# Kernel tuning notes

Measured on AMD Instinct MI355X. Metric: run time of the kernel, lower is better.

## Reference

```python
import jax, jax.numpy as jnp
import numpy as np
from jax import lax

B_, L_ = 2, 512
D_MODEL, EXPAND, HEAD_DIM, NGROUPS, D_STATE, D_CONV = 512, 2, 64, 1, 64, 3
D_INNER = EXPAND * D_MODEL            # 1024
NHEADS = D_INNER // HEAD_DIM          # 16
CONV_DIM = D_INNER + 2 * NGROUPS * D_STATE   # 1152
D_IN_PROJ = 2 * D_INNER + 2 * NGROUPS * D_STATE + NHEADS  # 2192
RMS_EPS = 1e-5


def silu(x):
    return x * jax.nn.sigmoid(x)


def segsum(x):
    # x: (..., T) -> (..., T, T); out[..., i, j] = sum_{j<k<=i} x[..., k], -inf above diag
    T = x.shape[-1]
    xr = jnp.broadcast_to(x[..., None], x.shape + (T,))
    keep = jnp.tril(jnp.ones((T, T), dtype=bool), -1)
    xr = jnp.where(keep, xr, 0.0)
    s = jnp.cumsum(xr, axis=-2)
    diag = jnp.tril(jnp.ones((T, T), dtype=bool), 0)
    return jnp.where(diag, s, -jnp.inf)


def ssd(x, A, Bm, Cm, chunk):
    # x: (b,l,h,p), A: (b,l,h), Bm/Cm: (b,l,g,n); chunk==1 as in the source forward
    b, l, h, p = x.shape
    c = l // chunk
    n = Bm.shape[-1]
    x = x.reshape(b, c, chunk, h, p)
    Bm = Bm.reshape(b, c, chunk, Bm.shape[2], n)
    Cm = Cm.reshape(b, c, chunk, Cm.shape[2], n)
    A = A.reshape(b, c, chunk, h).transpose(0, 3, 1, 2)        # (b,h,c,l)
    A_cumsum = jnp.cumsum(A, axis=-1)
    Lmat = jnp.exp(segsum(A))                                   # (b,h,c,l,l)
    # broadcast group dim (g==1) to heads, matching torch.einsum broadcasting
    Bb = jnp.broadcast_to(Bm, (b, c, chunk, h, n))
    Cb = jnp.broadcast_to(Cm, (b, c, chunk, h, n))
    Y_diag = jnp.einsum('bclhn,bcshn,bhcls,bcshp->bclhp', Cb, Bb, Lmat, x)
    decay_states = jnp.exp(A_cumsum[:, :, :, -1:] - A_cumsum)   # (b,h,c,l)
    states = jnp.einsum('bclhn,bhcl,bclhp->bchpn', Bb, decay_states, x)
    states = jnp.concatenate([jnp.zeros_like(states[:, :1]), states], axis=1)  # (b,c+1,h,p,n)
    A_last = jnp.pad(A_cumsum[:, :, :, -1], ((0, 0), (0, 0), (1, 0)))          # (b,h,c+1)
    decay_chunk = jnp.exp(segsum(A_last))                       # (b,h,c+1,c+1)
    new_states = jnp.einsum('bhzc,bchpn->bzhpn', decay_chunk, states)
    states = new_states[:, :-1]                                 # (b,c,h,p,n)
    state_decay_out = jnp.exp(A_cumsum)
    Y_off = jnp.einsum('bclhn,bchpn,bhcl->bclhp', Cb, states, state_decay_out)
    return (Y_diag + Y_off).reshape(b, l, h, p)


def causal_dwconv(x, w, bias):
    # x: (B,L,C); w: (C,K) depthwise; torch pads (K-1) both sides then slices [:L] == left-pad only
    xt = x.transpose(0, 2, 1)
    y = lax.conv_general_dilated(xt, w[:, None, :], (1,), [(D_CONV - 1, 0)],
                                 feature_group_count=CONV_DIM,
                                 dimension_numbers=('NCH', 'OIH', 'NCH'))
    return y.transpose(0, 2, 1) + bias


def setup_inputs() -> dict:
    key = jax.random.key(0)
    ks = jax.random.split(key, 8)
    u = jax.random.normal(ks[0], (B_, L_, D_MODEL), dtype=jnp.float32)
    W_in = jax.random.normal(ks[1], (D_MODEL, D_IN_PROJ), dtype=jnp.float32) / np.sqrt(D_MODEL).astype(np.float32)
    conv_w = jax.random.normal(ks[2], (CONV_DIM, D_CONV), dtype=jnp.float32) * 0.3
    conv_b = jnp.zeros((CONV_DIM,), dtype=jnp.float32)
    dt = jnp.exp(jax.random.uniform(ks[3], (NHEADS,), dtype=jnp.float32)
                 * (np.float32(np.log(0.1)) - np.float32(np.log(0.001))) + np.float32(np.log(0.001)))
    dt = jnp.clip(dt, 1e-4, None)
    dt_bias = dt + jnp.log(-jnp.expm1(-dt))
    A_log = jnp.log(jax.random.uniform(ks[4], (NHEADS,), dtype=jnp.float32, minval=1.0, maxval=16.0))
    D_param = jnp.ones((NHEADS,), dtype=jnp.float32)
    rms_w = jnp.ones((D_INNER,), dtype=jnp.float32)
    W_out = jax.random.normal(ks[5], (D_INNER, D_MODEL), dtype=jnp.float32) / np.sqrt(D_INNER).astype(np.float32)
    return {"u": u, "W_in": W_in, "conv_w": conv_w, "conv_b": conv_b, "dt_bias": dt_bias,
            "A_log": A_log, "D_param": D_param, "rms_w": rms_w, "W_out": W_out}


def reference(u, W_in, conv_w, conv_b, dt_bias, A_log, D_param, rms_w, W_out):
    b, l, _ = u.shape
    zxbcdt = u @ W_in                                   # (b,l,D_IN_PROJ)
    z = zxbcdt[..., :D_INNER]
    xBC = zxbcdt[..., D_INNER:D_INNER + CONV_DIM]
    dt = zxbcdt[..., D_INNER + CONV_DIM:]
    dt = jax.nn.softplus(dt + dt_bias)                  # (b,l,h)
    A = -jnp.exp(A_log)                                 # (h,)
    xBC = silu(causal_dwconv(xBC, conv_w, conv_b))      # (b,l,CONV_DIM)
    x = xBC[..., :D_INNER].reshape(b, l, NHEADS, HEAD_DIM)
    Bm = xBC[..., D_INNER:D_INNER + D_STATE][:, :, None, :]     # (b,l,1,n)
    Cm = xBC[..., D_INNER + D_STATE:][:, :, None, :]            # (b,l,1,n)
    y = ssd(x * dt[..., None], A * dt, Bm, Cm, 1)       # (b,l,h,p)
    y = y + x * D_param[:, None]
    y = y.reshape(b, l, D_INNER)
    # gated RMSNorm
    yz = y * silu(z)
    y = yz * lax.rsqrt(jnp.mean(yz * yz, axis=-1, keepdims=True) + RMS_EPS) * rms_w
    return y @ W_out
```

## Files before the change

### kernel.cpp

```cpp
#include <hip/hip_runtime.h>
#include <hip/hip_bf16.h>

#define B_SZ 2
#define L_SZ 512
#define D_MODEL 512
#define D_INNER 1024
#define HEAD_DIM 64
#define NHEADS 16
#define D_STATE 64
#define D_CONV 3
#define CONV_DIM 1152
#define D_IN_PROJ 2192
#define BL (B_SZ * L_SZ)
#define RMS_EPS 1e-5f
#define QC 64
#define NCH 8
#define NPAD1 2304
#define PB 72

typedef __attribute__((ext_vector_type(8))) short short8t;
typedef __attribute__((ext_vector_type(8))) unsigned short ushort8t;
typedef __attribute__((ext_vector_type(4))) unsigned short ushort4t;
typedef __attribute__((ext_vector_type(4))) float f32x4;

__device__ __forceinline__ unsigned short f2bf(float f) {
    unsigned u = __float_as_uint(f);
    u += 0x7fff + ((u >> 16) & 1);
    return (unsigned short)(u >> 16);
}
__device__ __forceinline__ float bf2f(unsigned short u) {
    return __uint_as_float(((unsigned)u) << 16);
}

__device__ __forceinline__ void gload_lds16(const void* g, void* lds) {
    __builtin_amdgcn_global_load_lds(
        (const __attribute__((address_space(1))) unsigned int*)g,
        (__attribute__((address_space(3))) unsigned int*)lds, 16, 0, 0);
}

__device__ __forceinline__ void transpose_tile_bf16(const float* __restrict__ src,
                                                    unsigned short* __restrict__ dst,
                                                    int K, int Nin, int tile, int ntn) {
    __shared__ float T[64][65];
    int tid = threadIdx.x;
    int nt = tile % ntn, kt = tile / ntn;
    int n0 = nt * 64, k0 = kt * 64;
#pragma unroll
    for (int rr = 0; rr < 4; ++rr) {
        int k = k0 + (tid >> 4) + rr * 16;
        int nn = (tid & 15) * 4;
#pragma unroll
        for (int q = 0; q < 4; ++q) {
            int n = n0 + nn + q;
            T[(tid >> 4) + rr * 16][nn + q] = (n < Nin) ? src[(size_t)k * Nin + n] : 0.f;
        }
    }
    __syncthreads();
    int nn2 = tid >> 2, kc = tid & 3;
    unsigned short ov[16];
#pragma unroll
    for (int j = 0; j < 16; ++j) ov[j] = f2bf(T[kc * 16 + j][nn2]);
    unsigned short* p = dst + (size_t)(n0 + nn2) * K + k0 + kc * 16;
    *(ushort8t*)p = *(ushort8t*)&ov[0];
    *(ushort8t*)(p + 8) = *(ushort8t*)&ov[8];
}

__global__ __launch_bounds__(256) void prep_kernel(const float* __restrict__ W_in,
                                                   const float* __restrict__ W_out,
                                                   const float* __restrict__ u,
                                                   unsigned short* __restrict__ Wt1,
                                                   unsigned short* __restrict__ Wt2,
                                                   unsigned short* __restrict__ u_bf) {
    int bid = blockIdx.x;
    if (bid < 288) {
        transpose_tile_bf16(W_in, Wt1, D_MODEL, D_IN_PROJ, bid, 36);
    } else if (bid < 416) {
        transpose_tile_bf16(W_out, Wt2, D_INNER, D_MODEL, bid - 288, 8);
    } else {
        int i = ((bid - 416) * 256 + threadIdx.x) * 8;
        float4 v0 = *(const float4*)(u + i);
        float4 v1 = *(const float4*)(u + i + 4);
        unsigned short ov[8] = {f2bf(v0.x), f2bf(v0.y), f2bf(v0.z), f2bf(v0.w),
                                f2bf(v1.x), f2bf(v1.y), f2bf(v1.z), f2bf(v1.w)};
        *(ushort8t*)(u_bf + i) = *(ushort8t*)&ov[0];
    }
}

__global__ __launch_bounds__(256) void gemm_in(const unsigned short* __restrict__ A,
                                               const unsigned short* __restrict__ Bt,
                                               float* __restrict__ C,
                                               unsigned short* __restrict__ xbc,
                                               float* __restrict__ dtb) {
    const int K = D_MODEL;
    __shared__ char sm[49152];
    int tid = threadIdx.x;
    int w = tid >> 6, l = tid & 63;
    int m0 = blockIdx.y * 64, n0 = blockIdx.x * 64;
    int wm = w >> 1, wn = w & 1;

    f32x4 acc[2][2];
#pragma unroll
    for (int i = 0; i < 2; ++i)
#pragma unroll
        for (int j = 0; j < 2; ++j) acc[i][j] = (f32x4){0.f, 0.f, 0.f, 0.f};

    auto stage = [&](const unsigned short* src, int row0, int k0, char* dst) {
#pragma unroll
        for (int p = 0; p < 2; ++p) {
            int c = w * 2 + p;
            int row = c * 8 + (l >> 3);
            int scb = ((l & 7) << 4) ^ ((row & 7) << 4);
            gload_lds16(src + (size_t)(row0 + row) * K + k0 + (scb >> 1), dst + c * 1024);
        }
    };

    const int nkt = K / 64;
    stage(A, m0, 0, sm);
    stage(Bt, n0, 0, sm + 8192);
    stage(A, m0, 64, sm + 16384);
    stage(Bt, n0, 64, sm + 16384 + 8192);

    for (int kt = 0; kt < nkt; ++kt) {
        if (kt + 2 < nkt) {
            char* d = sm + ((kt + 2) % 3) * 16384;
            stage(A, m0, (kt + 2) * 64, d);
            stage(Bt, n0, (kt + 2) * 64, d + 8192);
        }
        int inflight = nkt - 1 - kt;
        if (inflight >= 2)      asm volatile("s_waitcnt vmcnt(8)" ::: "memory");
        else if (inflight == 1) asm volatile("s_waitcnt vmcnt(4)" ::: "memory");
        else                    asm volatile("s_waitcnt vmcnt(0)" ::: "memory");
        __builtin_amdgcn_s_barrier();

        const char* Ab = sm + (kt % 3) * 16384;
        const char* Bb = Ab + 8192;
#pragma unroll
        for (int kk = 0; kk < 2; ++kk) {
            short8t af[2], bf[2];
#pragma unroll
            for (int i = 0; i < 2; ++i) {
                int r = wm * 32 + i * 16 + (l & 15);
                int cb = (kk * 64 + (l >> 4) * 16) ^ ((r & 7) << 4);
                af[i] = *(const short8t*)(Ab + r * 128 + cb);
            }
#pragma unroll
            for (int j = 0; j < 2; ++j) {
                int r = wn * 32 + j * 16 + (l & 15);
                int cb = (kk * 64 + (l >> 4) * 16) ^ ((r & 7) << 4);
                bf[j] = *(const short8t*)(Bb + r * 128 + cb);
            }
#pragma unroll
            for (int i = 0; i < 2; ++i)
#pragma unroll
                for (int j = 0; j < 2; ++j)
                    acc[i][j] = __builtin_amdgcn_mfma_f32_16x16x32_bf16(af[i], bf[j], acc[i][j], 0, 0, 0);
        }
        __builtin_amdgcn_s_barrier();
    }

#pragma unroll
    for (int i = 0; i < 2; ++i)
#pragma unroll
        for (int j = 0; j < 2; ++j) {
            int row = m0 + wm * 32 + i * 16 + (l >> 4) * 4;
            int col = n0 + wn * 32 + j * 16 + (l & 15);
#pragma unroll
            for (int r = 0; r < 4; ++r) {
                float v = acc[i][j][r];
                int rr = row + r;
                if (col < D_INNER) {
                    C[(size_t)rr * D_IN_PROJ + col] = v;
                } else if (col < D_INNER + CONV_DIM) {
                    xbc[(size_t)rr * CONV_DIM + (col - D_INNER)] = f2bf(v);
                } else if (col < D_IN_PROJ) {
                    dtb[(size_t)rr * 16 + (col - D_INNER - CONV_DIM)] = v;
                }
            }
        }
}

__device__ __forceinline__ float4 conv4b(const unsigned short* __restrict__ xrow,
                                         int gl, int ch,
                                         const float* __restrict__ conv_w,
                                         const float* __restrict__ conv_b) {
    ushort4t u2 = *(const ushort4t*)(xrow + ch);
    ushort4t u1 = {0, 0, 0, 0}, u0 = {0, 0, 0, 0};
    if (gl >= 1) u1 = *(const ushort4t*)(xrow + ch - CONV_DIM);
    if (gl >= 2) u0 = *(const ushort4t*)(xrow + ch - 2 * CONV_DIM);
    float4 o;
    float a;
    a = conv_b[ch+0] + conv_w[(ch+0)*3]*bf2f(u0[0]) + conv_w[(ch+0)*3+1]*bf2f(u1[0]) + conv_w[(ch+0)*3+2]*bf2f(u2[0]);
    o.x = a / (1.f + __expf(-a));
    a = conv_b[ch+1] + conv_w[(ch+1)*3]*bf2f(u0[1]) + conv_w[(ch+1)*3+1]*bf2f(u1[1]) + conv_w[(ch+1)*3+2]*bf2f(u2[1]);
    o.y = a / (1.f + __expf(-a));
    a = conv_b[ch+2] + conv_w[(ch+2)*3]*bf2f(u0[2]) + conv_w[(ch+2)*3+1]*bf2f(u1[2]) + conv_w[(ch+2)*3+2]*bf2f(u2[2]);
    o.z = a / (1.f + __expf(-a));
    a = conv_b[ch+3] + conv_w[(ch+3)*3]*bf2f(u0[3]) + conv_w[(ch+3)*3+1]*bf2f(u1[3]) + conv_w[(ch+3)*3+2]*bf2f(u2[3]);
    o.w = a / (1.f + __expf(-a));
    return o;
}

__global__ __launch_bounds__(256) void ssd_passA(const unsigned short* __restrict__ xbc,
                                                 const float* __restrict__ dtb,
                                                 const float* __restrict__ conv_w,
                                                 const float* __restrict__ conv_b,
                                                 const float* __restrict__ dt_bias,
                                                 const float* __restrict__ A_log,
                                                 const float* __restrict__ D_param,
                                                 float* __restrict__ y,
                                                 float* __restrict__ Zbuf,
                                                 float* __restrict__ Ebuf) {
    int blk = blockIdx.x;
    int h = blk & 15;
    int c = (blk >> 4) & 7;
    int b = blk >> 7;
    int tid = threadIdx.x;

    __shared__ __align__(16) unsigned short Cs_bf[QC][PB];
    __shared__ __align__(16) unsigned short Bs_bf[QC][PB];
    __shared__ __align__(16) unsigned short XDT_bf[QC][PB];
    __shared__ __align__(16) unsigned short BTw_bf[QC][PB];
    __shared__ float csh[QC], dts[QC], wh[QC];
#define PS_bf Cs_bf

    int bl0 = b * L_SZ + c * QC;

    if (tid < 64) {
        int t = tid;
        float draw = dtb[(size_t)(bl0 + t) * 16 + h];
        float dtv = draw + dt_bias[h];
        dtv = (dtv > 20.f) ? dtv : log1pf(expf(dtv));
        float A = -expf(A_log[h]);
        float cs = A * dtv;
#pragma unroll
        for (int off = 1; off < 64; off <<= 1) {
            float tmp = __shfl_up(cs, off);
            if (t >= off) cs += tmp;
        }
        float cs63 = __shfl(cs, 63);
        dts[t] = dtv;
        csh[t] = cs;
        wh[t] = __expf(cs63 - cs);
        Ebuf[(((size_t)(b * NHEADS + h) * NCH) + c) * QC + t] = __expf(cs);
    }

    int row16 = tid >> 4;
    int col4 = (tid & 15) * 4;
#pragma unroll
    for (int r = 0; r < 4; ++r) {
        int t = r * 16 + row16;
        int gl = c * QC + t;
        const unsigned short* xrow = xbc + (size_t)(bl0 + t) * CONV_DIM;
        float4 Bv = conv4b(xrow, gl, D_INNER + col4, conv_w, conv_b);
        float4 Cv = conv4b(xrow, gl, D_INNER + D_STATE + col4, conv_w, conv_b);
        ushort4t bq = {f2bf(Bv.x), f2bf(Bv.y), f2bf(Bv.z), f2bf(Bv.w)};
        ushort4t cq = {f2bf(Cv.x), f2bf(Cv.y), f2bf(Cv.z), f2bf(Cv.w)};
        *(ushort4t*)&Bs_bf[t][col4] = bq;
        *(ushort4t*)&Cs_bf[t][col4] = cq;
    }
    __syncthreads();

#pragma unroll
    for (int r = 0; r < 4; ++r) {
        int t = r * 16 + row16;
        int gl = c * QC + t;
        const unsigned short* xrow = xbc + (size_t)(bl0 + t) * CONV_DIM;
        float4 xv = conv4b(xrow, gl, h * HEAD_DIM + col4, conv_w, conv_b);
        float d = dts[t], wt = wh[t];
        xv.x *= d; xv.y *= d; xv.z *= d; xv.w *= d;
        ushort4t xq = {f2bf(xv.x), f2bf(xv.y), f2bf(xv.z), f2bf(xv.w)};
        ushort4t bq = *(ushort4t*)&Bs_bf[t][col4];
#pragma unroll
        for (int q = 0; q < 4; ++q) {
            int ch = col4 + q;
            int f8 = ((ch >> 2) & 7) << 3;
            XDT_bf[ch][t ^ f8] = xq[q];
            BTw_bf[ch][t ^ f8] = f2bf(bf2f(bq[q]) * wt);
        }
    }
    __syncthreads();

    int l = tid & 63, wv = tid >> 6;
    int wm = wv >> 1, wn = wv & 1;
    int fr = l & 15, fq = l >> 4;

    f32x4 g[2][2];
    {
#pragma unroll
        for (int i = 0; i < 2; ++i)
#pragma unroll
            for (int j = 0; j < 2; ++j) g[i][j] = (f32x4){0.f, 0.f, 0.f, 0.f};
#pragma unroll
        for (int kk = 0; kk < 2; ++kk) {
            short8t af[2], bb[2];
#pragma unroll
            for (int i = 0; i < 2; ++i)
                af[i] = *(const short8t*)&Cs_bf[wm * 32 + i * 16 + fr][kk * 32 + fq * 8];
#pragma unroll
            for (int j = 0; j < 2; ++j)
                bb[j] = *(const short8t*)&Bs_bf[wn * 32 + j * 16 + fr][kk * 32 + fq * 8];
#pragma unroll
            for (int i = 0; i < 2; ++i)
#pragma unroll
                for (int j = 0; j < 2; ++j)
                    g[i][j] = __builtin_amdgcn_mfma_f32_16x16x32_bf16(af[i], bb[j], g[i][j], 0, 0, 0);
        }
    }
    __syncthreads();

    {
#pragma unroll
        for (int i = 0; i < 2; ++i)
#pragma unroll
            for (int j = 0; j < 2; ++j) {
                int s = wn * 32 + j * 16 + fr;
                float css = csh[s];
#pragma unroll
                for (int r = 0; r < 4; ++r) {
                    int t = wm * 32 + i * 16 + fq * 4 + r;
                    float v = (s <= t) ? g[i][j][r] * __expf(csh[t] - css) : 0.f;
                    PS_bf[t][s] = f2bf(v);
                }
            }
    }
    __syncthreads();

    {
        f32x4 yv[2][2];
#pragma unroll
        for (int i = 0; i < 2; ++i)
#pragma unroll
            for (int j = 0; j < 2; ++j) yv[i][j] = (f32x4){0.f, 0.f, 0.f, 0.f};
#pragma unroll
        for (int kk = 0; kk < 2; ++kk) {
            short8t af[2], bb[2];
            int K0 = kk * 32 + fq * 8;
#pragma unroll
            for (int i = 0; i < 2; ++i)
                af[i] = *(const short8t*)&PS_bf[wm * 32 + i * 16 + fr][K0];
#pragma unroll
            for (int j = 0; j < 2; ++j) {
                int r = wn * 32 + j * 16 + fr;
                bb[j] = *(const short8t*)&XDT_bf[r][K0 ^ (((r >> 2) & 7) << 3)];
            }
#pragma unroll
            for (int i = 0; i < 2; ++i)
#pragma unroll
                for (int j = 0; j < 2; ++j)
                    yv[i][j] = __builtin_amdgcn_mfma_f32_16x16x32_bf16(af[i], bb[j], yv[i][j], 0, 0, 0);
        }
        float Dp = D_param[h];
#pragma unroll
        for (int i = 0; i < 2; ++i)
#pragma unroll
            for (int j = 0; j < 2; ++j) {
                int p = wn * 32 + j * 16 + fr;
                int f8 = ((p >> 2) & 7) << 3;
#pragma unroll
                for (int r = 0; r < 4; ++r) {
                    int t = wm * 32 + i * 16 + fq * 4 + r;
                    float xval = bf2f(XDT_bf[p][t ^ f8]);
                    float fct = Dp / dts[t];
                    y[(size_t)(bl0 + t) * D_INNER + h * HEAD_DIM + p] =
                        yv[i][j][r] + fct * xval;
                }
            }
    }

    {
        f32x4 zv[2][2];
#pragma unroll
        for (int i = 0; i < 2; ++i)
#pragma unroll
            for (int j = 0; j < 2; ++j) zv[i][j] = (f32x4){0.f, 0.f, 0.f, 0.f};
#pragma unroll
        for (int kk = 0; kk < 2; ++kk) {
            short8t af[2], bb[2];
            int K0 = kk * 32 + fq * 8;
#pragma unroll
            for (int i = 0; i < 2; ++i) {
                int r = wm * 32 + i * 16 + fr;
                af[i] = *(const short8t*)&XDT_bf[r][K0 ^ (((r >> 2) & 7) << 3)];
            }
#pragma unroll
            for (int j = 0; j < 2; ++j) {
                int r = wn * 32 + j * 16 + fr;
                bb[j] = *(const short8t*)&BTw_bf[r][K0 ^ (((r >> 2) & 7) << 3)];
            }
#pragma unroll
            for (int i = 0; i < 2; ++i)
#pragma unroll
                for (int j = 0; j < 2; ++j)
                    zv[i][j] = __builtin_amdgcn_mfma_f32_16x16x32_bf16(af[i], bb[j], zv[i][j], 0, 0, 0);
        }
        float* Zr = Zbuf + (((size_t)(b * NHEADS + h) * NCH) + c) * (HEAD_DIM * D_STATE);
#pragma unroll
        for (int i = 0; i < 2; ++i)
#pragma unroll
            for (int j = 0; j < 2; ++j) {
                int n = wn * 32 + j * 16 + fr;
#pragma unroll
                for (int r = 0; r < 4; ++r) {
                    int p = wm * 32 + i * 16 + fq * 4 + r;
                    Zr[p * D_STATE + n] = zv[i][j][r];
                }
            }
    }
#undef PS_bf
}

__global__ __launch_bounds__(256) void ssd_passC(const unsigned short* __restrict__ xbc,
                                                 const float* __restrict__ conv_w,
                                                 const float* __restrict__ conv_b,
                                                 const float* __restrict__ Zbuf,
                                                 const float* __restrict__ Ebuf,
                                                 float* __restrict__ y) {
    int blk = blockIdx.x;
    int h = blk & 15;
    int q = blk >> 4;
    int c = 1 + (q % 7);
    int b = q / 7;
    int tid = threadIdx.x;

    __shared__ __align__(16) unsigned short Cs_bf[QC][PB];
    __shared__ __align__(16) unsigned short S_bf[QC][PB];
    __shared__ float Eh[QC];

    int bl0 = b * L_SZ + c * QC;
    const float* Zb = Zbuf + ((size_t)(b * NHEADS + h) * NCH) * (HEAD_DIM * D_STATE);
    const float* Eb = Ebuf + ((size_t)(b * NHEADS + h) * NCH) * QC;

    {
        int p = tid >> 2, nq = (tid & 3) * 16;
        float S16[16];
#pragma unroll
        for (int qq = 0; qq < 16; ++qq) S16[qq] = 0.f;
        float wgt = 1.f;
        for (int j = c - 1; j >= 0; --j) {
            const float* Zj = Zb + (size_t)j * (HEAD_DIM * D_STATE) + p * D_STATE + nq;
#pragma unroll
            for (int q4 = 0; q4 < 4; ++q4) {
                float4 z = *(const float4*)(Zj + q4 * 4);
                S16[q4 * 4 + 0] += wgt * z.x;
                S16[q4 * 4 + 1] += wgt * z.y;
                S16[q4 * 4 + 2] += wgt * z.z;
                S16[q4 * 4 + 3] += wgt * z.w;
            }
            wgt *= Eb[(size_t)j * QC + 63];
        }
#pragma unroll
        for (int q4 = 0; q4 < 4; ++q4) {
            ushort4t s4 = {f2bf(S16[q4 * 4 + 0]), f2bf(S16[q4 * 4 + 1]),
                           f2bf(S16[q4 * 4 + 2]), f2bf(S16[q4 * 4 + 3])};
            *(ushort4t*)&S_bf[p][nq + q4 * 4] = s4;
        }
    }

    int row16 = tid >> 4, col4 = (tid & 15) * 4;
#pragma unroll
    for (int r = 0; r < 4; ++r) {
        int t = r * 16 + row16;
        int gl = c * QC + t;
        const unsigned short* xrow = xbc + (size_t)(bl0 + t) * CONV_DIM;
        float4 Cv = conv4b(xrow, gl, D_INNER + D_STATE + col4, conv_w, conv_b);
        ushort4t cq = {f2bf(Cv.x), f2bf(Cv.y), f2bf(Cv.z), f2bf(Cv.w)};
        *(ushort4t*)&Cs_bf[t][col4] = cq;
    }
    if (tid < 64)
        Eh[tid] = Ebuf[(((size_t)(b * NHEADS + h) * NCH) + c) * QC + tid];
    __syncthreads();

    int l = tid & 63, wv = tid >> 6;
    int wm = wv >> 1, wn = wv & 1;
    int fr = l & 15, fq = l >> 4;
    f32x4 acc[2][2];
#pragma unroll
    for (int i = 0; i < 2; ++i)
#pragma unroll
        for (int j = 0; j < 2; ++j) acc[i][j] = (f32x4){0.f, 0.f, 0.f, 0.f};
#pragma unroll
    for (int kk = 0; kk < 2; ++kk) {
        short8t af[2], bb[2];
#pragma unroll
        for (int i = 0; i < 2; ++i)
            af[i] = *(const short8t*)&Cs_bf[wm * 32 + i * 16 + fr][kk * 32 + fq * 8];
#pragma unroll
        for (int j = 0; j < 2; ++j)
            bb[j] = *(const short8t*)&S_bf[wn * 32 + j * 16 + fr][kk * 32 + fq * 8];
#pragma unroll
        for (int i = 0; i < 2; ++i)
#pragma unroll
            for (int j = 0; j < 2; ++j)
                acc[i][j] = __builtin_amdgcn_mfma_f32_16x16x32_bf16(af[i], bb[j], acc[i][j], 0, 0, 0);
    }
#pragma unroll
    for (int i = 0; i < 2; ++i)
#pragma unroll
        for (int j = 0; j < 2; ++j) {
            int p = wn * 32 + j * 16 + fr;
#pragma unroll
            for (int r = 0; r < 4; ++r) {
                int t = wm * 32 + i * 16 + fq * 4 + r;
                float* yp = y + (size_t)(bl0 + t) * D_INNER + h * HEAD_DIM + p;
                *yp += Eh[t] * acc[i][j][r];
            }
        }
}

__global__ __launch_bounds__(256) void gated_rmsnorm_kernel(const float* __restrict__ zxbcdt,
                                                            const float* __restrict__ y,
                                                            const float* __restrict__ rms_w,
                                                            unsigned short* __restrict__ yn_bf) {
    int bl = blockIdx.x;
    int tid = threadIdx.x;
    __shared__ float red[4];
    __shared__ float sscale;
    float vals[4];
    float sumsq = 0.f;
#pragma unroll
    for (int i = 0; i < 4; ++i) {
        int col = tid + i * 256;
        float yv = y[(size_t)bl * D_INNER + col];
        float z = zxbcdt[(size_t)bl * D_IN_PROJ + col];
        float yz = yv * (z / (1.f + expf(-z)));
        vals[i] = yz;
        sumsq += yz * yz;
    }
#pragma unroll
    for (int off = 32; off; off >>= 1) sumsq += __shfl_xor(sumsq, off);
    int wave = tid >> 6, lane = tid & 63;
    if (lane == 0) red[wave] = sumsq;
    __syncthreads();
    if (tid == 0) {
        float t = red[0] + red[1] + red[2] + red[3];
        sscale = rsqrtf(t / (float)D_INNER + RMS_EPS);
    }
    __syncthreads();
    float sc = sscale;
#pragma unroll
    for (int i = 0; i < 4; ++i) {
        int col = tid + i * 256;
        yn_bf[(size_t)bl * D_INNER + col] = f2bf(vals[i] * sc * rms_w[col]);
    }
}

__global__ __launch_bounds__(256) void gemm_mfma32(const unsigned short* __restrict__ A,
                                                   const unsigned short* __restrict__ Bt,
                                                   float* __restrict__ C,
                                                   int N, int K) {
    __shared__ char sm[36864];
    int tid = threadIdx.x;
    int w = tid >> 6, l = tid & 63;
    int m0 = blockIdx.y * 32, n0 = blockIdx.x * 64;
    int wm = w >> 1, wn = w & 1;

    f32x4 acc[2];
    acc[0] = (f32x4){0.f, 0.f, 0.f, 0.f};
    acc[1] = (f32x4){0.f, 0.f, 0.f, 0.f};

    auto stageA = [&](int k0, char* dst) {
        int row = w * 8 + (l >> 3);
        int scb = ((l & 7) << 4) ^ ((row & 7) << 4);
        gload_lds16(A + (size_t)(m0 + row) * K + k0 + (scb >> 1), dst + w * 1024);
    };
    auto stageB = [&](int k0, char* dst) {
#pragma unroll
        for (int p = 0; p < 2; ++p) {
            int c = w * 2 + p;
            int row = c * 8 + (l >> 3);
            int scb = ((l & 7) << 4) ^ ((row & 7) << 4);
            gload_lds16(Bt + (size_t)(n0 + row) * K + k0 + (scb >> 1), dst + c * 1024);
        }
    };

    int nkt = K / 64;
    stageA(0, sm); stageB(0, sm + 4096);
    stageA(64, sm + 12288); stageB(64, sm + 12288 + 4096);

    for (int kt = 0; kt < nkt; ++kt) {
        if (kt + 2 < nkt) {
            char* d = sm + ((kt + 2) % 3) * 12288;
            stageA((kt + 2) * 64, d);
            stageB((kt + 2) * 64, d + 4096);
        }
        int inflight = nkt - 1 - kt;
        if (inflight >= 2)      asm volatile("s_waitcnt vmcnt(6)" ::: "memory");
        else if (inflight == 1) asm volatile("s_waitcnt vmcnt(3)" ::: "memory");
        else                    asm volatile("s_waitcnt vmcnt(0)" ::: "memory");
        __builtin_amdgcn_s_barrier();

        const char* Ab = sm + (kt % 3) * 12288;
        const char* Bb = Ab + 4096;
#pragma unroll
        for (int kk = 0; kk < 2; ++kk) {
            short8t af;
            {
                int r = wm * 16 + (l & 15);
                int cb = (kk * 64 + (l >> 4) * 16) ^ ((r & 7) << 4);
                af = *(const short8t*)(Ab + r * 128 + cb);
            }
#pragma unroll
            for (int j = 0; j < 2; ++j) {
                int r = wn * 32 + j * 16 + (l & 15);
                int cb = (kk * 64 + (l >> 4) * 16) ^ ((r & 7) << 4);
                short8t bfv = *(const short8t*)(Bb + r * 128 + cb);
                acc[j] = __builtin_amdgcn_mfma_f32_16x16x32_bf16(af, bfv, acc[j], 0, 0, 0);
            }
        }
        __builtin_amdgcn_s_barrier();
    }

#pragma unroll
    for (int j = 0; j < 2; ++j) {
        int col = n0 + wn * 32 + j * 16 + (l & 15);
        int rowb = m0 + wm * 16 + (l >> 4) * 4;
#pragma unroll
        for (int r = 0; r < 4; ++r)
            C[(size_t)(rowb + r) * N + col] = acc[j][r];
    }
}

extern "C" void kernel_launch(void* const* d_in, const int* in_sizes, int n_in,
                              void* d_out, int out_size, void* d_ws, size_t ws_size,
                              hipStream_t stream) {
    const float* u       = (const float*)d_in[0];
    const float* W_in    = (const float*)d_in[1];
    const float* conv_w  = (const float*)d_in[2];
    const float* conv_b  = (const float*)d_in[3];
    const float* dt_bias = (const float*)d_in[4];
    const float* A_log   = (const float*)d_in[5];
    const float* D_param = (const float*)d_in[6];
    const float* rms_w   = (const float*)d_in[7];
    const float* W_out   = (const float*)d_in[8];
    float* out = (float*)d_out;

    float* ws = (float*)d_ws;
    float* zxbcdt = ws;
    float* y      = zxbcdt + (size_t)BL * D_IN_PROJ;
    float* Zbuf   = y + (size_t)BL * D_INNER;
    float* Ebuf   = Zbuf + (size_t)32 * NCH * 4096;
    float* dtb    = Ebuf + (size_t)32 * NCH * QC;
    unsigned short* u_bf  = (unsigned short*)(dtb + (size_t)BL * 16);
    unsigned short* Wt1   = u_bf + (size_t)BL * D_MODEL;
    unsigned short* Wt2   = Wt1 + (size_t)NPAD1 * D_MODEL;
    unsigned short* yn_bf = Wt2 + (size_t)D_MODEL * D_INNER;
    unsigned short* xbc   = yn_bf + (size_t)BL * D_INNER;

    prep_kernel<<<672, 256, 0, stream>>>(W_in, W_out, u, Wt1, Wt2, u_bf);

    gemm_in<<<dim3(NPAD1 / 64, BL / 64), 256, 0, stream>>>(
        u_bf, Wt1, zxbcdt, xbc, dtb);

    ssd_passA<<<B_SZ * NCH * NHEADS, 256, 0, stream>>>(
        xbc, dtb, conv_w, conv_b, dt_bias, A_log, D_param, y, Zbuf, Ebuf);
    ssd_passC<<<224, 256, 0, stream>>>(xbc, conv_w, conv_b, Zbuf, Ebuf, y);

    gated_rmsnorm_kernel<<<BL, 256, 0, stream>>>(zxbcdt, y, rms_w, yn_bf);

    gemm_mfma32<<<dim3(D_MODEL / 64, BL / 32), 256, 0, stream>>>(
        yn_bf, Wt2, out, D_MODEL, D_INNER);
}
```

Measured before the change: 47.19 us.

## Fuse gated RMSNorm into SSD epilogues and output GEMM row scaling

Removes the standalone gated RMSNorm kernel. The SSD pass epilogues now compute y*silu(z), write it as bf16 and emit per-head partial sums of squares. The output GEMM reduces those partials into a per-row rsqrt scale, and rms_w is folded into the transposed W_out during prep. This drops one launch and one full read/write of y, at the cost of extra z loads and reductions inside the SSD kernels and a small reduction in the GEMM epilogue.

```diff
diff --git a/kernel.cpp b/kernel.cpp
--- a/kernel.cpp
+++ b/kernel.cpp
@@ -39,6 +39,7 @@
 }
 
 __device__ __forceinline__ void transpose_tile_bf16(const float* __restrict__ src,
+                                                    const float* __restrict__ scale,
                                                     unsigned short* __restrict__ dst,
                                                     int K, int Nin, int tile, int ntn) {
     __shared__ float T[64][65];
@@ -48,11 +49,12 @@
 #pragma unroll
     for (int rr = 0; rr < 4; ++rr) {
         int k = k0 + (tid >> 4) + rr * 16;
+        float sc = scale ? scale[k] : 1.f;
         int nn = (tid & 15) * 4;
 #pragma unroll
         for (int q = 0; q < 4; ++q) {
             int n = n0 + nn + q;
-            T[(tid >> 4) + rr * 16][nn + q] = (n < Nin) ? src[(size_t)k * Nin + n] : 0.f;
+            T[(tid >> 4) + rr * 16][nn + q] = (n < Nin) ? src[(size_t)k * Nin + n] * sc : 0.f;
         }
     }
     __syncthreads();
@@ -67,15 +69,16 @@
 
 __global__ __launch_bounds__(256) void prep_kernel(const float* __restrict__ W_in,
                                                    const float* __restrict__ W_out,
+                                                   const float* __restrict__ rms_w,
                                                    const float* __restrict__ u,
                                                    unsigned short* __restrict__ Wt1,
                                                    unsigned short* __restrict__ Wt2,
                                                    unsigned short* __restrict__ u_bf) {
     int bid = blockIdx.x;
     if (bid < 288) {
-        transpose_tile_bf16(W_in, Wt1, D_MODEL, D_IN_PROJ, bid, 36);
+        transpose_tile_bf16(W_in, nullptr, Wt1, D_MODEL, D_IN_PROJ, bid, 36);
     } else if (bid < 416) {
-        transpose_tile_bf16(W_out, Wt2, D_INNER, D_MODEL, bid - 288, 8);
+        transpose_tile_bf16(W_out, rms_w, Wt2, D_INNER, D_MODEL, bid - 288, 8);
     } else {
         int i = ((bid - 416) * 256 + threadIdx.x) * 8;
         float4 v0 = *(const float4*)(u + i);
@@ -200,14 +203,19 @@
     return o;
 }
 
+__device__ __forceinline__ float silu(float z) { return z / (1.f + __expf(-z)); }
+
 __global__ __launch_bounds__(256) void ssd_passA(const unsigned short* __restrict__ xbc,
                                                  const float* __restrict__ dtb,
+                                                 const float* __restrict__ zx,
                                                  const float* __restrict__ conv_w,
                                                  const float* __restrict__ conv_b,
                                                  const float* __restrict__ dt_bias,
                                                  const float* __restrict__ A_log,
                                                  const float* __restrict__ D_param,
                                                  float* __restrict__ y,
+                                                 unsigned short* __restrict__ yz_bf,
+                                                 float* __restrict__ psum,
                                                  float* __restrict__ Zbuf,
                                                  float* __restrict__ Ebuf) {
     int blk = blockIdx.x;
@@ -221,6 +229,7 @@
     __shared__ __align__(16) unsigned short XDT_bf[QC][PB];
     __shared__ __align__(16) unsigned short BTw_bf[QC][PB];
     __shared__ float csh[QC], dts[QC], wh[QC];
+    __shared__ float sq_lds[QC][2];
 #define PS_bf Cs_bf
 
     int bl0 = b * L_SZ + c * QC;
@@ -350,21 +359,57 @@
                     yv[i][j] = __builtin_amdgcn_mfma_f32_16x16x32_bf16(af[i], bb[j], yv[i][j], 0, 0, 0);
         }
         float Dp = D_param[h];
-#pragma unroll
-        for (int i = 0; i < 2; ++i)
-#pragma unroll
-            for (int j = 0; j < 2; ++j) {
-                int p = wn * 32 + j * 16 + fr;
-                int f8 = ((p >> 2) & 7) << 3;
+        if (c == 0) {
+            float sloc[2][4] = {{0.f, 0.f, 0.f, 0.f}, {0.f, 0.f, 0.f, 0.f}};
+#pragma unroll
+            for (int i = 0; i < 2; ++i)
+#pragma unroll
+                for (int j = 0; j < 2; ++j) {
+                    int p = wn * 32 + j * 16 + fr;
+                    int f8 = ((p >> 2) & 7) << 3;
+#pragma unroll
+                    for (int r = 0; r < 4; ++r) {
+                        int t = wm * 32 + i * 16 + fq * 4 + r;
+                        float xval = bf2f(XDT_bf[p][t ^ f8]);
+                        float yval = yv[i][j][r] + (Dp / dts[t]) * xval;
+                        float z = zx[(size_t)(bl0 + t) * D_IN_PROJ + h * HEAD_DIM + p];
+                        float yz = yval * silu(z);
+                        yz_bf[(size_t)(bl0 + t) * D_INNER + h * HEAD_DIM + p] = f2bf(yz);
+                        sloc[i][r] += yz * yz;
+                    }
+                }
+#pragma unroll
+            for (int i = 0; i < 2; ++i)
 #pragma unroll
                 for (int r = 0; r < 4; ++r) {
-                    int t = wm * 32 + i * 16 + fq * 4 + r;
-                    float xval = bf2f(XDT_bf[p][t ^ f8]);
-                    float fct = Dp / dts[t];
-                    y[(size_t)(bl0 + t) * D_INNER + h * HEAD_DIM + p] =
-                        yv[i][j][r] + fct * xval;
+                    float v = sloc[i][r];
+                    v += __shfl_xor(v, 1); v += __shfl_xor(v, 2);
+                    v += __shfl_xor(v, 4); v += __shfl_xor(v, 8);
+                    if (fr == 0) {
+                        int t = wm * 32 + i * 16 + fq * 4 + r;
+                        sq_lds[t][wn] = v;
+                    }
                 }
-            }
+            __syncthreads();
+            if (tid < 64)
+                psum[(size_t)(bl0 + tid) * 16 + h] = sq_lds[tid][0] + sq_lds[tid][1];
+        } else {
+#pragma unroll
+            for (int i = 0; i < 2; ++i)
+#pragma unroll
+                for (int j = 0; j < 2; ++j) {
+                    int p = wn * 32 + j * 16 + fr;
+                    int f8 = ((p >> 2) & 7) << 3;
+#pragma unroll
+                    for (int r = 0; r < 4; ++r) {
+                        int t = wm * 32 + i * 16 + fq * 4 + r;
+                        float xval = bf2f(XDT_bf[p][t ^ f8]);
+                        float fct = Dp / dts[t];
+                        y[(size_t)(bl0 + t) * D_INNER + h * HEAD_DIM + p] =
+                            yv[i][j][r] + fct * xval;
+                    }
+                }
+        }
     }
 
     {
@@ -410,11 +455,14 @@
 }
 
 __global__ __launch_bounds__(256) void ssd_passC(const unsigned short* __restrict__ xbc,
+                                                 const float* __restrict__ zx,
                                                  const float* __restrict__ conv_w,
                                                  const float* __restrict__ conv_b,
                                                  const float* __restrict__ Zbuf,
                                                  const float* __restrict__ Ebuf,
-                                                 float* __restrict__ y) {
+                                                 const float* __restrict__ y,
+                                                 unsigned short* __restrict__ yz_bf,
+                                                 float* __restrict__ psum) {
     int blk = blockIdx.x;
     int h = blk & 15;
     int q = blk >> 4;
@@ -425,6 +473,7 @@
     __shared__ __align__(16) unsigned short Cs_bf[QC][PB];
     __shared__ __align__(16) unsigned short S_bf[QC][PB];
     __shared__ float Eh[QC];
+    __shared__ float sq_lds[QC][2];
 
     int bl0 = b * L_SZ + c * QC;
     const float* Zb = Zbuf + ((size_t)(b * NHEADS + h) * NCH) * (HEAD_DIM * D_STATE);
@@ -493,6 +542,8 @@
             for (int j = 0; j < 2; ++j)
                 acc[i][j] = __builtin_amdgcn_mfma_f32_16x16x32_bf16(af[i], bb[j], acc[i][j], 0, 0, 0);
     }
+
+    float sloc[2][4] = {{0.f, 0.f, 0.f, 0.f}, {0.f, 0.f, 0.f, 0.f}};
 #pragma unroll
     for (int i = 0; i < 2; ++i)
 #pragma unroll
@@ -501,54 +552,38 @@
 #pragma unroll
             for (int r = 0; r < 4; ++r) {
                 int t = wm * 32 + i * 16 + fq * 4 + r;
-                float* yp = y + (size_t)(bl0 + t) * D_INNER + h * HEAD_DIM + p;
-                *yp += Eh[t] * acc[i][j][r];
-            }
-        }
-}
-
-__global__ __launch_bounds__(256) void gated_rmsnorm_kernel(const float* __restrict__ zxbcdt,
-                                                            const float* __restrict__ y,
-                                                            const float* __restrict__ rms_w,
-                                                            unsigned short* __restrict__ yn_bf) {
-    int bl = blockIdx.x;
-    int tid = threadIdx.x;
-    __shared__ float red[4];
-    __shared__ float sscale;
-    float vals[4];
-    float sumsq = 0.f;
-#pragma unroll
-    for (int i = 0; i < 4; ++i) {
-        int col = tid + i * 256;
-        float yv = y[(size_t)bl * D_INNER + col];
-        float z = zxbcdt[(size_t)bl * D_IN_PROJ + col];
-        float yz = yv * (z / (1.f + expf(-z)));
-        vals[i] = yz;
-        sumsq += yz * yz;
-    }
-#pragma unroll
-    for (int off = 32; off; off >>= 1) sumsq += __shfl_xor(sumsq, off);
-    int wave = tid >> 6, lane = tid & 63;
-    if (lane == 0) red[wave] = sumsq;
+                size_t idx = (size_t)(bl0 + t) * D_INNER + h * HEAD_DIM + p;
+                float yval = y[idx] + Eh[t] * acc[i][j][r];
+                float z = zx[(size_t)(bl0 + t) * D_IN_PROJ + h * HEAD_DIM + p];
+                float yz = yval * silu(z);
+                yz_bf[idx] = f2bf(yz);
+                sloc[i][r] += yz * yz;
+            }
+        }
+#pragma unroll
+    for (int i = 0; i < 2; ++i)
+#pragma unroll
+        for (int r = 0; r < 4; ++r) {
+            float v = sloc[i][r];
+            v += __shfl_xor(v, 1); v += __shfl_xor(v, 2);
+            v += __shfl_xor(v, 4); v += __shfl_xor(v, 8);
+            if (fr == 0) {
+                int t = wm * 32 + i * 16 + fq * 4 + r;
+                sq_lds[t][wn] = v;
+            }
+        }
     __syncthreads();
-    if (tid == 0) {
-        float t = red[0] + red[1] + red[2] + red[3];
-        sscale = rsqrtf(t / (float)D_INNER + RMS_EPS);
-    }
-    __syncthreads();
-    float sc = sscale;
-#pragma unroll
-    for (int i = 0; i < 4; ++i) {
-        int col = tid + i * 256;
-        yn_bf[(size_t)bl * D_INNER + col] = f2bf(vals[i] * sc * rms_w[col]);
-    }
-}
-
-__global__ __launch_bounds__(256) void gemm_mfma32(const unsigned short* __restrict__ A,
-                                                   const unsigned short* __restrict__ Bt,
-                                                   float* __restrict__ C,
-                                                   int N, int K) {
+    if (tid < 64)
+        psum[(size_t)(bl0 + tid) * 16 + h] = sq_lds[tid][0] + sq_lds[tid][1];
+}
+
+__global__ __launch_bounds__(256) void gemm_out(const unsigned short* __restrict__ A,
+                                                const unsigned short* __restrict__ Bt,
+                                                const float* __restrict__ psum,
+                                                float* __restrict__ C) {
+    const int N = D_MODEL, K = D_INNER;
     __shared__ char sm[36864];
+    __shared__ float scl[32];
     int tid = threadIdx.x;
     int w = tid >> 6, l = tid & 63;
     int m0 = blockIdx.y * 32, n0 = blockIdx.x * 64;
@@ -573,7 +608,7 @@
         }
     };
 
-    int nkt = K / 64;
+    const int nkt = K / 64;
     stageA(0, sm); stageB(0, sm + 4096);
     stageA(64, sm + 12288); stageB(64, sm + 12288 + 4096);
 
@@ -610,13 +645,22 @@
         __builtin_amdgcn_s_barrier();
     }
 
+    if (tid < 32) {
+        const float* pr = psum + (size_t)(m0 + tid) * 16;
+        float s = 0.f;
+#pragma unroll
+        for (int qq = 0; qq < 16; ++qq) s += pr[qq];
+        scl[tid] = rsqrtf(s / (float)D_INNER + RMS_EPS);
+    }
+    __syncthreads();
+
 #pragma unroll
     for (int j = 0; j < 2; ++j) {
         int col = n0 + wn * 32 + j * 16 + (l & 15);
-        int rowb = m0 + wm * 16 + (l >> 4) * 4;
+        int rloc = wm * 16 + (l >> 4) * 4;
 #pragma unroll
         for (int r = 0; r < 4; ++r)
-            C[(size_t)(rowb + r) * N + col] = acc[j][r];
+            C[(size_t)(m0 + rloc + r) * N + col] = acc[j][r] * scl[rloc + r];
     }
 }
 
@@ -640,23 +684,24 @@
     float* Zbuf   = y + (size_t)BL * D_INNER;
     float* Ebuf   = Zbuf + (size_t)32 * NCH * 4096;
     float* dtb    = Ebuf + (size_t)32 * NCH * QC;
-    unsigned short* u_bf  = (unsigned short*)(dtb + (size_t)BL * 16);
+    float* psum   = dtb + (size_t)BL * 16;
+    unsigned short* u_bf  = (unsigned short*)(psum + (size_t)BL * 16);
     unsigned short* Wt1   = u_bf + (size_t)BL * D_MODEL;
     unsigned short* Wt2   = Wt1 + (size_t)NPAD1 * D_MODEL;
-    unsigned short* yn_bf = Wt2 + (size_t)D_MODEL * D_INNER;
-    unsigned short* xbc   = yn_bf + (size_t)BL * D_INNER;
-
-    prep_kernel<<<672, 256, 0, stream>>>(W_in, W_out, u, Wt1, Wt2, u_bf);
+    unsigned short* yz_bf = Wt2 + (size_t)D_MODEL * D_INNER;
+    unsigned short* xbc   = yz_bf + (size_t)BL * D_INNER;
+
+    prep_kernel<<<672, 256, 0, stream>>>(W_in, W_out, rms_w, u, Wt1, Wt2, u_bf);
 
     gemm_in<<<dim3(NPAD1 / 64, BL / 64), 256, 0, stream>>>(
         u_bf, Wt1, zxbcdt, xbc, dtb);
 
     ssd_passA<<<B_SZ * NCH * NHEADS, 256, 0, stream>>>(
-        xbc, dtb, conv_w, conv_b, dt_bias, A_log, D_param, y, Zbuf, Ebuf);
-    ssd_passC<<<224, 256, 0, stream>>>(xbc, conv_w, conv_b, Zbuf, Ebuf, y);
-
-    gated_rmsnorm_kernel<<<BL, 256, 0, stream>>>(zxbcdt, y, rms_w, yn_bf);
-
-    gemm_mfma32<<<dim3(D_MODEL / 64, BL / 32), 256, 0, stream>>>(
-        yn_bf, Wt2, out, D_MODEL, D_INNER);
-}
+        xbc, dtb, zxbcdt, conv_w, conv_b, dt_bias, A_log, D_param,
+        y, yz_bf, psum, Zbuf, Ebuf);
+    ssd_passC<<<224, 256, 0, stream>>>(
+        xbc, zxbcdt, conv_w, conv_b, Zbuf, Ebuf, y, yz_bf, psum);
+
+    gemm_out<<<dim3(D_MODEL / 64, BL / 32), 256, 0, stream>>>(
+        yz_bf, Wt2, psum, out);
+}
```

Result: no change. 47.15 us (-0.1%).
